# Performance work log

Hardware: AMD Instinct MI355X
Metric: run time of the kernel (lower is better)

The kernel has to match this reference:

```python
import jax, jax.numpy as jnp
import numpy as np

NUM_HEADS = 32
ROPE_BASE = 10000.0


def _rope_tables(seq_len, dim):
    inv_freq = 1.0 / (ROPE_BASE ** (jnp.arange(0, dim, 2, dtype=jnp.float32) / dim))
    t = jnp.arange(seq_len, dtype=jnp.float32)
    freqs = jnp.outer(t, inv_freq)                      # [S, dim/2]
    emb = jnp.concatenate([freqs, freqs], axis=-1)      # [S, dim]
    return jnp.cos(emb), jnp.sin(emb)


def _rotate_half(x):
    x1, x2 = jnp.split(x, 2, axis=-1)
    return jnp.concatenate([-x2, x1], axis=-1)


def setup_inputs() -> dict:
    key = jax.random.key(0)
    ks = jax.random.split(key, 5)
    B, T, C = 1, 4096, 4096
    hidden_states = jax.random.normal(ks[0], (B, T, C), dtype=jnp.float32)
    position_ids = jnp.arange(B * T, dtype=jnp.int64 if jax.config.jax_enable_x64 else jnp.int32).reshape(B, T)
    s = 0.02
    Wq = jax.random.normal(ks[1], (C, C), dtype=jnp.float32) * s
    Wk = jax.random.normal(ks[2], (C, C), dtype=jnp.float32) * s
    Wv = jax.random.normal(ks[3], (C, C), dtype=jnp.float32) * s
    Wo = jax.random.normal(ks[4], (C, C), dtype=jnp.float32) * s
    return {"hidden_states": hidden_states, "position_ids": position_ids,
            "Wq": Wq, "Wk": Wk, "Wv": Wv, "Wo": Wo}


def reference(hidden_states, position_ids, Wq, Wk, Wv, Wo):
    B, T, C = hidden_states.shape
    nh = NUM_HEADS
    hs = C // nh

    # Projections (torch Linear: x @ W.T), split heads -> [B, nh, T, hs]
    q = (hidden_states @ Wq.T).reshape(B, T, nh, hs).transpose(0, 2, 1, 3)
    k = (hidden_states @ Wk.T).reshape(B, T, nh, hs).transpose(0, 2, 1, 3)
    v = (hidden_states @ Wv.T).reshape(B, T, nh, hs).transpose(0, 2, 1, 3)

    # RoPE (prefill: kv_len == T)
    cos, sin = _rope_tables(T, hs)                      # [T, hs]
    cos_b = cos[position_ids][:, None]                  # [B, 1, T, hs]
    sin_b = sin[position_ids][:, None]
    q = q * cos_b + _rotate_half(q) * sin_b
    k = k * cos_b + _rotate_half(k) * sin_b

    # Eager attention with full [B, nh, T, T] scores (faithful to source)
    scale = hs ** -0.5
    attn = jnp.einsum("bhqd,bhkd->bhqk", q, k) * scale
    causal = jnp.tril(jnp.ones((T, T), dtype=bool))     # diagonal = kv_len - T = 0
    attn = jnp.where(causal[None, None], attn, -jnp.inf)
    attn = jax.nn.softmax(attn, axis=-1)
    out = jnp.einsum("bhqk,bhkd->bhqd", attn, v)
    out = out.transpose(0, 2, 1, 3).reshape(B, T, C)
    return out @ Wo.T
```

## Files before the change

### kernel.cpp

```cpp
#include <hip/hip_runtime.h>

typedef __attribute__((ext_vector_type(8))) short short8;
typedef __attribute__((ext_vector_type(4))) short short4v;
typedef __attribute__((ext_vector_type(4))) float f32x4;

#define NH 32
#define HS 128
#define CDIM 4096
#define QBLK 256
#define KVBLK 64
#define NQT 16

__device__ __forceinline__ ushort f2bf(float f) {
  union { float f; unsigned u; } a; a.f = f;
  unsigned u = a.u;
  return (ushort)((u + 0x7FFFu + ((u >> 16) & 1u)) >> 16);
}
__device__ __forceinline__ float bf2f(ushort h) {
  union { unsigned u; float f; } a; a.u = ((unsigned)h) << 16;
  return a.f;
}
__device__ __forceinline__ unsigned cvtpk_bf16(float lo, float hi) {
  unsigned r;
  asm("v_cvt_pk_bf16_f32 %0, %1, %2" : "=v"(r) : "v"(lo), "v"(hi));
  return r;
}

__device__ __forceinline__ void gld16(const void* g, void* l) {
  __builtin_amdgcn_global_load_lds((const __attribute__((address_space(1))) void*)g,
                                   (__attribute__((address_space(3))) void*)l, 16, 0, 0);
}

__device__ __forceinline__ unsigned lds_off(const void* p) {
  return (unsigned)(uintptr_t)(const __attribute__((address_space(3))) void*)p;
}

template<int OFF>
__device__ __forceinline__ short4v ds_tr16(unsigned addr) {
  short4v r;
  asm volatile("ds_read_b64_tr_b16 %0, %1 offset:%c2" : "=v"(r) : "v"(addr), "i"(OFF));
  return r;
}

__global__ __launch_bounds__(256) void cast_bf16_kernel(const float* __restrict__ in,
                                                        ushort* __restrict__ out, int n4) {
  int i = blockIdx.x * 256 + threadIdx.x;
  if (i >= n4) return;
  float4 v = ((const float4*)in)[i];
  ushort4 o;
  o.x = f2bf(v.x); o.y = f2bf(v.y); o.z = f2bf(v.z); o.w = f2bf(v.w);
  ((ushort4*)out)[i] = o;
}

#define A00 0
#define A01 16384
#define A10 32768
#define A11 49152
#define B00 65536
#define B01 81920
#define B10 98304
#define B11 114688

template<typename OutT>
__global__ __launch_bounds__(512, 2) void gemm256(const ushort* __restrict__ A,
                                                  const ushort* __restrict__ B,
                                                  OutT* __restrict__ C) {
  __shared__ char sm[131072];
  const int tid = threadIdx.x;
  const int w = tid >> 6, lane = tid & 63, lhi = lane >> 4, llo = lane & 15;

  const int bid = blockIdx.x;
  const int x = (bid & 7) * 32 + (bid >> 3);
  const int mt = x >> 4, nt = x & 15;
  const size_t m0 = (size_t)mt * 256, n0 = (size_t)nt * 256;

  const char* A0p = (const char*)(A + m0 * 4096);
  const char* A1p = A0p + 1048576;
  const char* B0p = (const char*)(B + n0 * 4096);
  const char* B1p = B0p + 1048576;

  const int i0 = tid, i1 = tid + 512;
  const int ri0 = i0 >> 3, ri1 = i1 >> 3;
  const int cg0 = (i0 & 7) ^ (((ri0 >> 2) & 1) << 1);
  const int cg1 = (i1 & 7) ^ (((ri1 >> 2) & 1) << 1);
  const int off0 = ri0 * 8192 + cg0 * 16;
  const int off1 = ri1 * 8192 + cg1 * 16;
  const unsigned sd0 = (unsigned)(w * 1024);
  const unsigned sd1 = (unsigned)(8192 + w * 1024);

  const int sw = ((llo >> 2) & 1) << 1;
  const unsigned rd0 = (unsigned)((llo * 8 + ((0 * 4 + lhi) ^ sw)) * 16);
  const unsigned rd1 = (unsigned)((llo * 8 + ((1 * 4 + lhi) ^ sw)) * 16);

  const int wmg = w >> 2, wng = w & 3;
  const unsigned aE = wmg ? A01 : A00;
  const unsigned aO = wmg ? A11 : A10;
  const unsigned bE = (wng >> 1) ? B01 : B00;
  const unsigned bO = (wng >> 1) ? B11 : B10;
  const unsigned bco = (unsigned)((wng & 1) * 8192);

  f32x4 acc[8][4] = {};
  short8 a0[4], a1[4], u0[2], u1[2], v0[2], v1[2];

#define STG(PAN, K0, LB) do { \
    gld16((PAN) + (size_t)(K0) * 2 + off0, sm + (LB) + sd0); \
    gld16((PAN) + (size_t)(K0) * 2 + off1, sm + (LB) + sd1); \
  } while (0)
#define LDA(BASE, MQ) do { _Pragma("unroll") for (int m_ = 0; m_ < 4; m_++) { \
    a0[m_] = *(const short8*)(sm + (BASE) + (MQ) * 8192 + m_ * 2048 + rd0); \
    a1[m_] = *(const short8*)(sm + (BASE) + (MQ) * 8192 + m_ * 2048 + rd1); } } while (0)
#define LDB(R0, R1, BASE, NQ) do { _Pragma("unroll") for (int n_ = 0; n_ < 2; n_++) { \
    R0[n_] = *(const short8*)(sm + (BASE) + bco + (NQ) * 4096 + n_ * 2048 + rd0); \
    R1[n_] = *(const short8*)(sm + (BASE) + bco + (NQ) * 4096 + n_ * 2048 + rd1); } } while (0)
#define MM(MQ, NQ, R0, R1) do { \
    _Pragma("unroll") for (int m_ = 0; m_ < 4; m_++) _Pragma("unroll") for (int n_ = 0; n_ < 2; n_++) \
      acc[(MQ) * 4 + m_][(NQ) * 2 + n_] = __builtin_amdgcn_mfma_f32_16x16x32_bf16(a0[m_], R0[n_], acc[(MQ) * 4 + m_][(NQ) * 2 + n_], 0, 0, 0); \
    _Pragma("unroll") for (int m_ = 0; m_ < 4; m_++) _Pragma("unroll") for (int n_ = 0; n_ < 2; n_++) \
      acc[(MQ) * 4 + m_][(NQ) * 2 + n_] = __builtin_amdgcn_mfma_f32_16x16x32_bf16(a1[m_], R1[n_], acc[(MQ) * 4 + m_][(NQ) * 2 + n_], 0, 0, 0); \
  } while (0)
#define BAR1 do { __builtin_amdgcn_s_barrier(); \
    asm volatile("s_waitcnt lgkmcnt(0)" ::: "memory"); \
    __builtin_amdgcn_sched_barrier(0); \
    __builtin_amdgcn_s_setprio(1); } while (0)
#define BAR2 do { __builtin_amdgcn_s_setprio(0); __builtin_amdgcn_s_barrier(); \
    __builtin_amdgcn_sched_barrier(0); } while (0)

  STG(B0p, 0, B00); STG(B1p, 0, B01); STG(A0p, 0, A00); STG(A1p, 0, A01);
  STG(B0p, 64, B10); STG(B1p, 64, B11); STG(A0p, 64, A10); STG(A1p, 64, A11);
  asm volatile("s_waitcnt vmcnt(8)" ::: "memory");
  __builtin_amdgcn_s_barrier();
  __builtin_amdgcn_sched_barrier(0);

  for (int it = 0; it < 32; ++it) {
    const int kc = it * 128;
    const bool st = (it < 31);
    LDA(aE, 0); LDB(u0, u1, bE, 0);
    BAR1; MM(0, 0, u0, u1); BAR2;
    LDB(v0, v1, bE, 1);
    BAR1; MM(0, 1, v0, v1); BAR2;
    LDA(aE, 1);
    if (st) STG(B0p, kc + 128, B00);
    BAR1; MM(1, 1, v0, v1); BAR2;
    if (st) { STG(B1p, kc + 128, B01); STG(A0p, kc + 128, A00); }
    BAR1; MM(1, 0, u0, u1);
    __builtin_amdgcn_s_setprio(0);
    if (st) asm volatile("s_waitcnt vmcnt(6)" ::: "memory");
    else    asm volatile("s_waitcnt vmcnt(0)" ::: "memory");
    __builtin_amdgcn_s_barrier();
    __builtin_amdgcn_sched_barrier(0);
    LDA(aO, 0); LDB(u0, u1, bO, 0);
    if (st) STG(A1p, kc + 128, A01);
    BAR1; MM(0, 0, u0, u1); BAR2;
    LDB(v0, v1, bO, 1);
    BAR1; MM(0, 1, v0, v1); BAR2;
    LDA(aO, 1);
    if (st) { STG(B0p, kc + 192, B10); STG(B1p, kc + 192, B11); }
    BAR1; MM(1, 1, v0, v1); BAR2;
    if (st) { STG(A0p, kc + 192, A10); STG(A1p, kc + 192, A11); }
    BAR1; MM(1, 0, u0, u1);
    __builtin_amdgcn_s_setprio(0);
    if (st) asm volatile("s_waitcnt vmcnt(8)" ::: "memory");
    __builtin_amdgcn_s_barrier();
    __builtin_amdgcn_sched_barrier(0);
  }

  const int wm = wmg * 128, wn = wng * 64;
#pragma unroll
  for (int m = 0; m < 8; m++) {
#pragma unroll
    for (int nf = 0; nf < 4; nf++) {
      const size_t col = n0 + wn + nf * 16 + llo;
#pragma unroll
      for (int j = 0; j < 4; j++) {
        const size_t row = m0 + wm + m * 16 + lhi * 4 + j;
        if constexpr (sizeof(OutT) == 4)
          C[row * 4096 + col] = acc[m][nf][j];
        else
          C[row * 4096 + col] = f2bf(acc[m][nf][j]);
      }
    }
  }
#undef STG
#undef LDA
#undef LDB
#undef MM
#undef BAR1
#undef BAR2
}

__global__ __launch_bounds__(256) void rope_kernel(ushort* __restrict__ Q,
                                                   ushort* __restrict__ Kb,
                                                   const int* __restrict__ pos_ids,
                                                   int nrows) {
  int gid = blockIdx.x * 256 + threadIdx.x;
  int d = gid & 63;
  int row = gid >> 6;
  if (row >= nrows) return;
  int t = row >> 5;
  int pos = pos_ids[t];
  float inv = expf((float)d * -0.14391156831212788f);
  float ang = (float)pos * inv;
  float s, c;
  sincosf(ang, &s, &c);
  size_t base = (size_t)row * HS;
  {
    float x1 = bf2f(Q[base + d]), x2 = bf2f(Q[base + d + 64]);
    Q[base + d]      = f2bf(x1 * c - x2 * s);
    Q[base + d + 64] = f2bf(x2 * c + x1 * s);
  }
  {
    float x1 = bf2f(Kb[base + d]), x2 = bf2f(Kb[base + d + 64]);
    Kb[base + d]      = f2bf(x1 * c - x2 * s);
    Kb[base + d + 64] = f2bf(x2 * c + x1 * s);
  }
}

__global__ __launch_bounds__(512) void flash_attn(const ushort* __restrict__ Q,
                                                  const ushort* __restrict__ K,
                                                  const ushort* __restrict__ V,
                                                  ushort* __restrict__ O) {
  __shared__ __align__(16) ushort Ks[KVBLK * HS];
  __shared__ __align__(16) ushort Vs[KVBLK * HS];
  __shared__ __align__(16) ushort Ps[8][32 * 72];
  const int tid = threadIdx.x;
  const int w = tid >> 6, l = tid & 63, lhi = l >> 4, llo = l & 15;
  const int qbp = blockIdx.x, h = blockIdx.y;

  const int g = llo >> 2, c = llo & 3;
  const int swz = g | ((lhi & 1) << 2);
  const int c1 = c >> 1;
  const int swL = swz & 1, swH = swz & 6;
  const unsigned trbase = lds_off(Vs) + (unsigned)((lhi * 8 + g) * 256 + ((c1 ^ swL) << 4) + (c & 1) * 8);

  const int srow = tid >> 4, sch = tid & 15;
  const int schK = sch ^ (srow & 7);
  const int schV = sch ^ ((srow & 3) | (((srow >> 3) & 1) << 2));

  char* pwB = (char*)Ps[w];
  const float scale = 0.08838834764831845f;

  short8 kreg[2], vreg[2];

  for (int ph = 0; ph < 2; ph++) {
    const int qt = ph ? (NQT - 1 - qbp) : qbp;
    const int qr0 = qt * QBLK + w * 32;
    const int ntile = 4 * qt + 4;

    short8 aq[2][4];
#pragma unroll
    for (int mf = 0; mf < 2; mf++) {
      const ushort* qp = Q + (size_t)(qr0 + mf * 16 + llo) * CDIM + h * HS + lhi * 8;
#pragma unroll
      for (int ki = 0; ki < 4; ki++) aq[mf][ki] = *(const short8*)(qp + ki * 32);
    }

    f32x4 acc[2][8] = {};
    float mrow[2] = {-1e30f, -1e30f};
    float lrow[2] = {0.f, 0.f};

#pragma unroll
    for (int r = 0; r < 2; r++) {
      const size_t rb = (size_t)(srow + r * 32) * CDIM + h * HS + sch * 8;
      kreg[r] = *(const short8*)(K + rb);
      vreg[r] = *(const short8*)(V + rb);
    }
#pragma unroll
    for (int r = 0; r < 2; r++) {
      const int row = srow + r * 32;
      *(short8*)((char*)Ks + ((row * 16 + schK) << 4)) = kreg[r];
      *(short8*)((char*)Vs + ((row * 16 + schV) << 4)) = vreg[r];
    }
    __syncthreads();

    for (int t = 0; t < ntile; t++) {
      const int kv0 = t * KVBLK;
      if (t + 1 < ntile) {
        const size_t rb = (size_t)(kv0 + KVBLK + srow) * CDIM + h * HS + sch * 8;
#pragma unroll
        for (int r = 0; r < 2; r++) {
          kreg[r] = *(const short8*)(K + rb + (size_t)r * 32 * CDIM);
          vreg[r] = *(const short8*)(V + rb + (size_t)r * 32 * CDIM);
        }
      }
      const bool active = (kv0 <= qr0 + 31);
      if (active) {
        f32x4 s[2][4];
        __builtin_amdgcn_s_setprio(1);
#pragma unroll
        for (int nt = 0; nt < 4; nt++) {
          const int krow = nt * 16 + llo;
          const char* kr = (const char*)Ks + krow * 256;
          short8 kf[4];
#pragma unroll
          for (int ki = 0; ki < 4; ki++)
            kf[ki] = *(const short8*)(kr + (((ki * 4 + lhi) ^ (krow & 7)) << 4));
          f32x4 s0 = {0.f, 0.f, 0.f, 0.f}, s1 = {0.f, 0.f, 0.f, 0.f};
#pragma unroll
          for (int ki = 0; ki < 4; ki++) {
            s0 = __builtin_amdgcn_mfma_f32_16x16x32_bf16(kf[ki], aq[0][ki], s0, 0, 0, 0);
            s1 = __builtin_amdgcn_mfma_f32_16x16x32_bf16(kf[ki], aq[1][ki], s1, 0, 0, 0);
          }
          s[0][nt] = s0; s[1][nt] = s1;
        }
        __builtin_amdgcn_s_setprio(0);

        short4v vl0[8], vh0[8];
#pragma unroll
        for (int on = 0; on < 8; on++) {
          unsigned a = trbase + (unsigned)(((on * 2) ^ swH) << 4);
          vl0[on] = ds_tr16<0>(a);
          vh0[on] = ds_tr16<1024>(a);
        }

        const bool needm = (kv0 + KVBLK - 1 > qr0);
#pragma unroll
        for (int mf = 0; mf < 2; mf++) {
          const int qi = qr0 + mf * 16 + llo;
#pragma unroll
          for (int nt = 0; nt < 4; nt++) {
            const int kvb = kv0 + nt * 16 + lhi * 4;
#pragma unroll
            for (int j = 0; j < 4; j++) {
              float sv = s[mf][nt][j] * scale;
              if (needm && kvb + j > qi) sv = -1e30f;
              s[mf][nt][j] = sv;
            }
          }
        }

#pragma unroll
        for (int mf = 0; mf < 2; mf++) {
          f32x4 mm;
#pragma unroll
          for (int j = 0; j < 4; j++)
            mm[j] = fmaxf(fmaxf(s[mf][0][j], s[mf][1][j]), fmaxf(s[mf][2][j], s[mf][3][j]));
          float pmax = fmaxf(fmaxf(mm[0], mm[1]), fmaxf(mm[2], mm[3]));
          pmax = fmaxf(pmax, __shfl_xor(pmax, 16));
          pmax = fmaxf(pmax, __shfl_xor(pmax, 32));
          if (__any(pmax > mrow[mf] + 8.f)) {
            float mn = fmaxf(mrow[mf], pmax);
            float sc = __expf(mrow[mf] - mn);
            mrow[mf] = mn;
            lrow[mf] *= sc;
#pragma unroll
            for (int on = 0; on < 8; on++)
#pragma unroll
              for (int j = 0; j < 4; j++) acc[mf][on][j] *= sc;
          }
          float rs = 0.f;
#pragma unroll
          for (int nt = 0; nt < 4; nt++) {
            float p0 = __expf(s[mf][nt][0] - mrow[mf]);
            float p1 = __expf(s[mf][nt][1] - mrow[mf]);
            float p2 = __expf(s[mf][nt][2] - mrow[mf]);
            float p3 = __expf(s[mf][nt][3] - mrow[mf]);
            rs += (p0 + p1) + (p2 + p3);
            uint2 pk;
            pk.x = cvtpk_bf16(p0, p1);
            pk.y = cvtpk_bf16(p2, p3);
            *(uint2*)(pwB + (mf * 16 + llo) * 144 + nt * 32 + lhi * 8) = pk;
          }
          rs += __shfl_xor(rs, 16);
          rs += __shfl_xor(rs, 32);
          lrow[mf] += rs;
        }

        {
          short8 pf0 = *(const short8*)(pwB + llo * 144 + lhi * 16);
          short8 pf1 = *(const short8*)(pwB + (16 + llo) * 144 + lhi * 16);
          asm volatile("s_waitcnt lgkmcnt(0)" ::: "memory");
          __builtin_amdgcn_sched_barrier(0);
          __builtin_amdgcn_s_setprio(1);
#pragma unroll
          for (int on = 0; on < 8; on++) {
            short8 vf = __builtin_shufflevector(vl0[on], vh0[on], 0, 1, 2, 3, 4, 5, 6, 7);
            acc[0][on] = __builtin_amdgcn_mfma_f32_16x16x32_bf16(vf, pf0, acc[0][on], 0, 0, 0);
            acc[1][on] = __builtin_amdgcn_mfma_f32_16x16x32_bf16(vf, pf1, acc[1][on], 0, 0, 0);
          }
          __builtin_amdgcn_s_setprio(0);
        }
        {
          short8 pf0 = *(const short8*)(pwB + llo * 144 + 64 + lhi * 16);
          short8 pf1 = *(const short8*)(pwB + (16 + llo) * 144 + 64 + lhi * 16);
          short4v vl[8], vh[8];
#pragma unroll
          for (int on = 0; on < 8; on++) {
            unsigned a = trbase + (unsigned)(((on * 2) ^ swH) << 4);
            vl[on] = ds_tr16<8192>(a);
            vh[on] = ds_tr16<9216>(a);
          }
          asm volatile("s_waitcnt lgkmcnt(0)" ::: "memory");
          __builtin_amdgcn_sched_barrier(0);
          __builtin_amdgcn_s_setprio(1);
#pragma unroll
          for (int on = 0; on < 8; on++) {
            short8 vf = __builtin_shufflevector(vl[on], vh[on], 0, 1, 2, 3, 4, 5, 6, 7);
            acc[0][on] = __builtin_amdgcn_mfma_f32_16x16x32_bf16(vf, pf0, acc[0][on], 0, 0, 0);
            acc[1][on] = __builtin_amdgcn_mfma_f32_16x16x32_bf16(vf, pf1, acc[1][on], 0, 0, 0);
          }
          __builtin_amdgcn_s_setprio(0);
        }
      }

      __syncthreads();
      if (t + 1 < ntile) {
#pragma unroll
        for (int r = 0; r < 2; r++) {
          const int row = srow + r * 32;
          *(short8*)((char*)Ks + ((row * 16 + schK) << 4)) = kreg[r];
          *(short8*)((char*)Vs + ((row * 16 + schV) << 4)) = vreg[r];
        }
      }
      __syncthreads();
    }

#pragma unroll
    for (int mf = 0; mf < 2; mf++) {
      const float ri = 1.0f / lrow[mf];
      ushort* orow = O + (size_t)(qr0 + mf * 16 + llo) * CDIM + h * HS + lhi * 4;
#pragma unroll
      for (int on = 0; on < 8; on++) {
        ushort4 o4;
        o4.x = f2bf(acc[mf][on][0] * ri);
        o4.y = f2bf(acc[mf][on][1] * ri);
        o4.z = f2bf(acc[mf][on][2] * ri);
        o4.w = f2bf(acc[mf][on][3] * ri);
        *(ushort4*)(orow + on * 16) = o4;
      }
    }
  }
}

extern "C" void kernel_launch(void* const* d_in, const int* in_sizes, int n_in,
                              void* d_out, int out_size, void* d_ws, size_t ws_size,
                              hipStream_t stream) {
  const float* hs = (const float*)d_in[0];
  const int* pos = (const int*)d_in[1];
  const float* Wq = (const float*)d_in[2];
  const float* Wk = (const float*)d_in[3];
  const float* Wv = (const float*)d_in[4];
  const float* Wo = (const float*)d_in[5];
  float* out = (float*)d_out;

  const int T = 4096;
  const size_t elems = (size_t)T * CDIM;

  ushort* hsb  = (ushort*)d_ws;
  ushort* wbuf = hsb + elems;
  ushort* qb   = wbuf + elems;
  ushort* kb   = qb + elems;
  ushort* vb   = kb + elems;
  ushort* attn = hsb;

  const int n4 = (int)(elems / 4);
  const int castBlocks = (n4 + 255) / 256;

  cast_bf16_kernel<<<castBlocks, 256, 0, stream>>>(hs, hsb, n4);

  cast_bf16_kernel<<<castBlocks, 256, 0, stream>>>(Wq, wbuf, n4);
  gemm256<ushort><<<256, 512, 0, stream>>>(hsb, wbuf, qb);

  cast_bf16_kernel<<<castBlocks, 256, 0, stream>>>(Wk, wbuf, n4);
  gemm256<ushort><<<256, 512, 0, stream>>>(hsb, wbuf, kb);

  cast_bf16_kernel<<<castBlocks, 256, 0, stream>>>(Wv, wbuf, n4);
  gemm256<ushort><<<256, 512, 0, stream>>>(hsb, wbuf, vb);

  rope_kernel<<<(T * NH * 64) / 256, 256, 0, stream>>>(qb, kb, pos, T * NH);

  flash_attn<<<dim3(NQT / 2, NH), 512, 0, stream>>>(qb, kb, vb, attn);

  cast_bf16_kernel<<<castBlocks, 256, 0, stream>>>(Wo, wbuf, n4);
  gemm256<float><<<256, 512, 0, stream>>>(attn, wbuf, out);
}
```

Measured before the change: 830.0 us.

## Split flash attention KV range across two blocks and merge with combine kernel

Flash attention now launches twice as many blocks along a new z dimension. Each block handles alternating KV tiles and writes its unnormalised partial output plus per-row max and sum statistics. A new combine kernel then merges the two partials with log-sum-exp weights, and the output buffer is reused as scratch space. This is meant to raise occupancy, since the grid of 256 blocks underfills the GPU, at the cost of extra global traffic, an extra launch, and bf16 rounding of the partial results. The GEMM also drops several sched_barrier calls, giving the compiler more scheduling freedom.

```diff
diff --git a/kernel.cpp b/kernel.cpp
--- a/kernel.cpp
+++ b/kernel.cpp
@@ -122,8 +122,7 @@
     asm volatile("s_waitcnt lgkmcnt(0)" ::: "memory"); \
     __builtin_amdgcn_sched_barrier(0); \
     __builtin_amdgcn_s_setprio(1); } while (0)
-#define BAR2 do { __builtin_amdgcn_s_setprio(0); __builtin_amdgcn_s_barrier(); \
-    __builtin_amdgcn_sched_barrier(0); } while (0)
+#define BAR2 do { __builtin_amdgcn_s_setprio(0); __builtin_amdgcn_s_barrier(); } while (0)
 
   STG(B0p, 0, B00); STG(B1p, 0, B01); STG(A0p, 0, A00); STG(A1p, 0, A01);
   STG(B0p, 64, B10); STG(B1p, 64, B11); STG(A0p, 64, A10); STG(A1p, 64, A11);
@@ -147,7 +146,6 @@
     if (st) asm volatile("s_waitcnt vmcnt(6)" ::: "memory");
     else    asm volatile("s_waitcnt vmcnt(0)" ::: "memory");
     __builtin_amdgcn_s_barrier();
-    __builtin_amdgcn_sched_barrier(0);
     LDA(aO, 0); LDB(u0, u1, bO, 0);
     if (st) STG(A1p, kc + 128, A01);
     BAR1; MM(0, 0, u0, u1); BAR2;
@@ -161,7 +159,6 @@
     __builtin_amdgcn_s_setprio(0);
     if (st) asm volatile("s_waitcnt vmcnt(8)" ::: "memory");
     __builtin_amdgcn_s_barrier();
-    __builtin_amdgcn_sched_barrier(0);
   }
 
   const int wm = wmg * 128, wn = wng * 64;
@@ -218,13 +215,18 @@
 __global__ __launch_bounds__(512) void flash_attn(const ushort* __restrict__ Q,
                                                   const ushort* __restrict__ K,
                                                   const ushort* __restrict__ V,
-                                                  ushort* __restrict__ O) {
+                                                  ushort* __restrict__ O0,
+                                                  ushort* __restrict__ O1,
+                                                  float2* __restrict__ ml0,
+                                                  float2* __restrict__ ml1) {
   __shared__ __align__(16) ushort Ks[KVBLK * HS];
   __shared__ __align__(16) ushort Vs[KVBLK * HS];
   __shared__ __align__(16) ushort Ps[8][32 * 72];
   const int tid = threadIdx.x;
   const int w = tid >> 6, l = tid & 63, lhi = l >> 4, llo = l & 15;
-  const int qbp = blockIdx.x, h = blockIdx.y;
+  const int qbp = blockIdx.x, h = blockIdx.y, z = blockIdx.z;
+  ushort* __restrict__ Op = z ? O1 : O0;
+  float2* __restrict__ mlp = z ? ml1 : ml0;
 
   const int g = llo >> 2, c = llo & 3;
   const int swz = g | ((lhi & 1) << 2);
@@ -260,7 +262,7 @@
 
 #pragma unroll
     for (int r = 0; r < 2; r++) {
-      const size_t rb = (size_t)(srow + r * 32) * CDIM + h * HS + sch * 8;
+      const size_t rb = (size_t)(z * KVBLK + srow + r * 32) * CDIM + h * HS + sch * 8;
       kreg[r] = *(const short8*)(K + rb);
       vreg[r] = *(const short8*)(V + rb);
     }
@@ -272,10 +274,10 @@
     }
     __syncthreads();
 
-    for (int t = 0; t < ntile; t++) {
+    for (int t = z; t < ntile; t += 2) {
       const int kv0 = t * KVBLK;
-      if (t + 1 < ntile) {
-        const size_t rb = (size_t)(kv0 + KVBLK + srow) * CDIM + h * HS + sch * 8;
+      if (t + 2 < ntile) {
+        const size_t rb = (size_t)(kv0 + 2 * KVBLK + srow) * CDIM + h * HS + sch * 8;
 #pragma unroll
         for (int r = 0; r < 2; r++) {
           kreg[r] = *(const short8*)(K + rb + (size_t)r * 32 * CDIM);
@@ -403,7 +405,7 @@
       }
 
       __syncthreads();
-      if (t + 1 < ntile) {
+      if (t + 2 < ntile) {
 #pragma unroll
         for (int r = 0; r < 2; r++) {
           const int row = srow + r * 32;
@@ -416,19 +418,47 @@
 
 #pragma unroll
     for (int mf = 0; mf < 2; mf++) {
-      const float ri = 1.0f / lrow[mf];
-      ushort* orow = O + (size_t)(qr0 + mf * 16 + llo) * CDIM + h * HS + lhi * 4;
+      const int q = qr0 + mf * 16 + llo;
+      if (lhi == 0) {
+        float2 v2; v2.x = mrow[mf]; v2.y = lrow[mf];
+        mlp[(size_t)h * 4096 + q] = v2;
+      }
+      ushort* orow = Op + (size_t)q * CDIM + h * HS + lhi * 4;
 #pragma unroll
       for (int on = 0; on < 8; on++) {
         ushort4 o4;
-        o4.x = f2bf(acc[mf][on][0] * ri);
-        o4.y = f2bf(acc[mf][on][1] * ri);
-        o4.z = f2bf(acc[mf][on][2] * ri);
-        o4.w = f2bf(acc[mf][on][3] * ri);
+        o4.x = f2bf(acc[mf][on][0]);
+        o4.y = f2bf(acc[mf][on][1]);
+        o4.z = f2bf(acc[mf][on][2]);
+        o4.w = f2bf(acc[mf][on][3]);
         *(ushort4*)(orow + on * 16) = o4;
       }
     }
   }
+}
+
+__global__ __launch_bounds__(256) void combine_kernel(ushort* __restrict__ O0,
+                                                      const ushort* __restrict__ O1,
+                                                      const float2* __restrict__ ml0,
+                                                      const float2* __restrict__ ml1) {
+  int cch = blockIdx.x * 256 + threadIdx.x;
+  int q = cch >> 9;
+  int h = (cch >> 4) & 31;
+  int x = cch & 15;
+  size_t off = (size_t)q * CDIM + h * HS + x * 8;
+  float2 a = ml0[h * 4096 + q];
+  float2 b = ml1[h * 4096 + q];
+  float m = fmaxf(a.x, b.x);
+  float w0 = __expf(a.x - m), w1 = __expf(b.x - m);
+  float inv = 1.0f / (w0 * a.y + w1 * b.y);
+  w0 *= inv; w1 *= inv;
+  short8 u = *(const short8*)(O0 + off);
+  short8 v = *(const short8*)(O1 + off);
+  short8 r;
+#pragma unroll
+  for (int j = 0; j < 8; j++)
+    r[j] = (short)f2bf(bf2f((ushort)u[j]) * w0 + bf2f((ushort)v[j]) * w1);
+  *(short8*)(O0 + off) = r;
 }
 
 extern "C" void kernel_launch(void* const* d_in, const int* in_sizes, int n_in,
@@ -450,7 +480,10 @@
   ushort* qb   = wbuf + elems;
   ushort* kb   = qb + elems;
   ushort* vb   = kb + elems;
-  ushort* attn = hsb;
+
+  ushort* O1  = (ushort*)d_out;
+  float2* ml0 = (float2*)((char*)d_out + 33554432);
+  float2* ml1 = ml0 + (size_t)NH * T;
 
   const int n4 = (int)(elems / 4);
   const int castBlocks = (n4 + 255) / 256;
@@ -468,8 +501,9 @@
 
   rope_kernel<<<(T * NH * 64) / 256, 256, 0, stream>>>(qb, kb, pos, T * NH);
 
-  flash_attn<<<dim3(NQT / 2, NH), 512, 0, stream>>>(qb, kb, vb, attn);
+  flash_attn<<<dim3(NQT / 2, NH, 2), 512, 0, stream>>>(qb, kb, vb, hsb, O1, ml0, ml1);
+  combine_kernel<<<(T * NH * 16) / 256, 256, 0, stream>>>(hsb, O1, ml0, ml1);
 
   cast_bf16_kernel<<<castBlocks, 256, 0, stream>>>(Wo, wbuf, n4);
-  gemm256<float><<<256, 512, 0, stream>>>(attn, wbuf, out);
-}
+  gemm256<float><<<256, 512, 0, stream>>>(hsb, wbuf, out);
+}
```

Result: slower. 859.6 us (+3.6%).

## Use 16 waves of 16 query rows in flash attention, relax GEMM sched barriers

Applied to the files above, without the earlier changes.

The flash attention kernel moves from 8 waves each handling 32 query rows to 16 waves (1024 threads) each handling 16 rows. Each thread now loads a single K/V row chunk into LDS per tile. This raises the wave count per block and lowers register pressure per wave, at the cost of reusing each loaded K/V fragment over fewer query rows. Separately, several sched_barrier fences in the GEMM main loop are removed so the compiler can reorder instructions around the barriers.

```diff
diff --git a/kernel.cpp b/kernel.cpp
--- a/kernel.cpp
+++ b/kernel.cpp
@@ -122,8 +122,7 @@
     asm volatile("s_waitcnt lgkmcnt(0)" ::: "memory"); \
     __builtin_amdgcn_sched_barrier(0); \
     __builtin_amdgcn_s_setprio(1); } while (0)
-#define BAR2 do { __builtin_amdgcn_s_setprio(0); __builtin_amdgcn_s_barrier(); \
-    __builtin_amdgcn_sched_barrier(0); } while (0)
+#define BAR2 do { __builtin_amdgcn_s_setprio(0); __builtin_amdgcn_s_barrier(); } while (0)
 
   STG(B0p, 0, B00); STG(B1p, 0, B01); STG(A0p, 0, A00); STG(A1p, 0, A01);
   STG(B0p, 64, B10); STG(B1p, 64, B11); STG(A0p, 64, A10); STG(A1p, 64, A11);
@@ -147,7 +146,6 @@
     if (st) asm volatile("s_waitcnt vmcnt(6)" ::: "memory");
     else    asm volatile("s_waitcnt vmcnt(0)" ::: "memory");
     __builtin_amdgcn_s_barrier();
-    __builtin_amdgcn_sched_barrier(0);
     LDA(aO, 0); LDB(u0, u1, bO, 0);
     if (st) STG(A1p, kc + 128, A01);
     BAR1; MM(0, 0, u0, u1); BAR2;
@@ -161,7 +159,6 @@
     __builtin_amdgcn_s_setprio(0);
     if (st) asm volatile("s_waitcnt vmcnt(8)" ::: "memory");
     __builtin_amdgcn_s_barrier();
-    __builtin_amdgcn_sched_barrier(0);
   }
 
   const int wm = wmg * 128, wn = wng * 64;
@@ -215,13 +212,13 @@
   }
 }
 
-__global__ __launch_bounds__(512) void flash_attn(const ushort* __restrict__ Q,
-                                                  const ushort* __restrict__ K,
-                                                  const ushort* __restrict__ V,
-                                                  ushort* __restrict__ O) {
+__global__ __launch_bounds__(1024) void flash_attn(const ushort* __restrict__ Q,
+                                                   const ushort* __restrict__ K,
+                                                   const ushort* __restrict__ V,
+                                                   ushort* __restrict__ O) {
   __shared__ __align__(16) ushort Ks[KVBLK * HS];
   __shared__ __align__(16) ushort Vs[KVBLK * HS];
-  __shared__ __align__(16) ushort Ps[8][32 * 72];
+  __shared__ __align__(16) ushort Ps[16][16 * 72];
   const int tid = threadIdx.x;
   const int w = tid >> 6, l = tid & 63, lhi = l >> 4, llo = l & 15;
   const int qbp = blockIdx.x, h = blockIdx.y;
@@ -239,36 +236,30 @@
   char* pwB = (char*)Ps[w];
   const float scale = 0.08838834764831845f;
 
-  short8 kreg[2], vreg[2];
+  short8 kreg, vreg;
 
   for (int ph = 0; ph < 2; ph++) {
     const int qt = ph ? (NQT - 1 - qbp) : qbp;
-    const int qr0 = qt * QBLK + w * 32;
+    const int qr0 = qt * QBLK + w * 16;
     const int ntile = 4 * qt + 4;
 
-    short8 aq[2][4];
-#pragma unroll
-    for (int mf = 0; mf < 2; mf++) {
-      const ushort* qp = Q + (size_t)(qr0 + mf * 16 + llo) * CDIM + h * HS + lhi * 8;
-#pragma unroll
-      for (int ki = 0; ki < 4; ki++) aq[mf][ki] = *(const short8*)(qp + ki * 32);
+    short8 aq[4];
+    {
+      const ushort* qp = Q + (size_t)(qr0 + llo) * CDIM + h * HS + lhi * 8;
+#pragma unroll
+      for (int ki = 0; ki < 4; ki++) aq[ki] = *(const short8*)(qp + ki * 32);
     }
 
-    f32x4 acc[2][8] = {};
-    float mrow[2] = {-1e30f, -1e30f};
-    float lrow[2] = {0.f, 0.f};
-
-#pragma unroll
-    for (int r = 0; r < 2; r++) {
-      const size_t rb = (size_t)(srow + r * 32) * CDIM + h * HS + sch * 8;
-      kreg[r] = *(const short8*)(K + rb);
-      vreg[r] = *(const short8*)(V + rb);
-    }
-#pragma unroll
-    for (int r = 0; r < 2; r++) {
-      const int row = srow + r * 32;
-      *(short8*)((char*)Ks + ((row * 16 + schK) << 4)) = kreg[r];
-      *(short8*)((char*)Vs + ((row * 16 + schV) << 4)) = vreg[r];
+    f32x4 acc[8] = {};
+    float mrow = -1e30f;
+    float lrow = 0.f;
+
+    {
+      const size_t rb = (size_t)srow * CDIM + h * HS + sch * 8;
+      kreg = *(const short8*)(K + rb);
+      vreg = *(const short8*)(V + rb);
+      *(short8*)((char*)Ks + ((srow * 16 + schK) << 4)) = kreg;
+      *(short8*)((char*)Vs + ((srow * 16 + schV) << 4)) = vreg;
     }
     __syncthreads();
 
@@ -276,15 +267,12 @@
       const int kv0 = t * KVBLK;
       if (t + 1 < ntile) {
         const size_t rb = (size_t)(kv0 + KVBLK + srow) * CDIM + h * HS + sch * 8;
-#pragma unroll
-        for (int r = 0; r < 2; r++) {
-          kreg[r] = *(const short8*)(K + rb + (size_t)r * 32 * CDIM);
-          vreg[r] = *(const short8*)(V + rb + (size_t)r * 32 * CDIM);
-        }
+        kreg = *(const short8*)(K + rb);
+        vreg = *(const short8*)(V + rb);
       }
-      const bool active = (kv0 <= qr0 + 31);
+      const bool active = (kv0 <= qr0 + 15);
       if (active) {
-        f32x4 s[2][4];
+        f32x4 s[4];
         __builtin_amdgcn_s_setprio(1);
 #pragma unroll
         for (int nt = 0; nt < 4; nt++) {
@@ -294,94 +282,84 @@
 #pragma unroll
           for (int ki = 0; ki < 4; ki++)
             kf[ki] = *(const short8*)(kr + (((ki * 4 + lhi) ^ (krow & 7)) << 4));
-          f32x4 s0 = {0.f, 0.f, 0.f, 0.f}, s1 = {0.f, 0.f, 0.f, 0.f};
-#pragma unroll
-          for (int ki = 0; ki < 4; ki++) {
-            s0 = __builtin_amdgcn_mfma_f32_16x16x32_bf16(kf[ki], aq[0][ki], s0, 0, 0, 0);
-            s1 = __builtin_amdgcn_mfma_f32_16x16x32_bf16(kf[ki], aq[1][ki], s1, 0, 0, 0);
-          }
-          s[0][nt] = s0; s[1][nt] = s1;
+          f32x4 s0 = {0.f, 0.f, 0.f, 0.f};
+#pragma unroll
+          for (int ki = 0; ki < 4; ki++)
+            s0 = __builtin_amdgcn_mfma_f32_16x16x32_bf16(kf[ki], aq[ki], s0, 0, 0, 0);
+          s[nt] = s0;
         }
         __builtin_amdgcn_s_setprio(0);
 
-        short4v vl0[8], vh0[8];
-#pragma unroll
-        for (int on = 0; on < 8; on++) {
-          unsigned a = trbase + (unsigned)(((on * 2) ^ swH) << 4);
-          vl0[on] = ds_tr16<0>(a);
-          vh0[on] = ds_tr16<1024>(a);
+        const bool needm = (kv0 + KVBLK - 1 > qr0);
+        const int qi = qr0 + llo;
+#pragma unroll
+        for (int nt = 0; nt < 4; nt++) {
+          const int kvb = kv0 + nt * 16 + lhi * 4;
+#pragma unroll
+          for (int j = 0; j < 4; j++) {
+            float sv = s[nt][j] * scale;
+            if (needm && kvb + j > qi) sv = -1e30f;
+            s[nt][j] = sv;
+          }
         }
 
-        const bool needm = (kv0 + KVBLK - 1 > qr0);
-#pragma unroll
-        for (int mf = 0; mf < 2; mf++) {
-          const int qi = qr0 + mf * 16 + llo;
-#pragma unroll
-          for (int nt = 0; nt < 4; nt++) {
-            const int kvb = kv0 + nt * 16 + lhi * 4;
-#pragma unroll
-            for (int j = 0; j < 4; j++) {
-              float sv = s[mf][nt][j] * scale;
-              if (needm && kvb + j > qi) sv = -1e30f;
-              s[mf][nt][j] = sv;
-            }
-          }
-        }
-
-#pragma unroll
-        for (int mf = 0; mf < 2; mf++) {
+        {
           f32x4 mm;
 #pragma unroll
           for (int j = 0; j < 4; j++)
-            mm[j] = fmaxf(fmaxf(s[mf][0][j], s[mf][1][j]), fmaxf(s[mf][2][j], s[mf][3][j]));
+            mm[j] = fmaxf(fmaxf(s[0][j], s[1][j]), fmaxf(s[2][j], s[3][j]));
           float pmax = fmaxf(fmaxf(mm[0], mm[1]), fmaxf(mm[2], mm[3]));
           pmax = fmaxf(pmax, __shfl_xor(pmax, 16));
           pmax = fmaxf(pmax, __shfl_xor(pmax, 32));
-          if (__any(pmax > mrow[mf] + 8.f)) {
-            float mn = fmaxf(mrow[mf], pmax);
-            float sc = __expf(mrow[mf] - mn);
-            mrow[mf] = mn;
-            lrow[mf] *= sc;
+          if (__any(pmax > mrow + 8.f)) {
+            float mn = fmaxf(mrow, pmax);
+            float sc = __expf(mrow - mn);
+            mrow = mn;
+            lrow *= sc;
 #pragma unroll
             for (int on = 0; on < 8; on++)
 #pragma unroll
-              for (int j = 0; j < 4; j++) acc[mf][on][j] *= sc;
+              for (int j = 0; j < 4; j++) acc[on][j] *= sc;
           }
           float rs = 0.f;
 #pragma unroll
           for (int nt = 0; nt < 4; nt++) {
-            float p0 = __expf(s[mf][nt][0] - mrow[mf]);
-            float p1 = __expf(s[mf][nt][1] - mrow[mf]);
-            float p2 = __expf(s[mf][nt][2] - mrow[mf]);
-            float p3 = __expf(s[mf][nt][3] - mrow[mf]);
+            float p0 = __expf(s[nt][0] - mrow);
+            float p1 = __expf(s[nt][1] - mrow);
+            float p2 = __expf(s[nt][2] - mrow);
+            float p3 = __expf(s[nt][3] - mrow);
             rs += (p0 + p1) + (p2 + p3);
             uint2 pk;
             pk.x = cvtpk_bf16(p0, p1);
             pk.y = cvtpk_bf16(p2, p3);
-            *(uint2*)(pwB + (mf * 16 + llo) * 144 + nt * 32 + lhi * 8) = pk;
+            *(uint2*)(pwB + llo * 144 + nt * 32 + lhi * 8) = pk;
           }
           rs += __shfl_xor(rs, 16);
           rs += __shfl_xor(rs, 32);
-          lrow[mf] += rs;
+          lrow += rs;
         }
 
         {
-          short8 pf0 = *(const short8*)(pwB + llo * 144 + lhi * 16);
-          short8 pf1 = *(const short8*)(pwB + (16 + llo) * 144 + lhi * 16);
+          short8 pf = *(const short8*)(pwB + llo * 144 + lhi * 16);
+          short4v vl[8], vh[8];
+#pragma unroll
+          for (int on = 0; on < 8; on++) {
+            unsigned a = trbase + (unsigned)(((on * 2) ^ swH) << 4);
+            vl[on] = ds_tr16<0>(a);
+            vh[on] = ds_tr16<1024>(a);
+          }
           asm volatile("s_waitcnt lgkmcnt(0)" ::: "memory");
           __builtin_amdgcn_sched_barrier(0);
           __builtin_amdgcn_s_setprio(1);
 #pragma unroll
           for (int on = 0; on < 8; on++) {
-            short8 vf = __builtin_shufflevector(vl0[on], vh0[on], 0, 1, 2, 3, 4, 5, 6, 7);
-            acc[0][on] = __builtin_amdgcn_mfma_f32_16x16x32_bf16(vf, pf0, acc[0][on], 0, 0, 0);
-            acc[1][on] = __builtin_amdgcn_mfma_f32_16x16x32_bf16(vf, pf1, acc[1][on], 0, 0, 0);
+            short8 vf = __builtin_shufflevector(vl[on], vh[on], 0, 1, 2, 3, 4, 5, 6, 7);
+            acc[on] = __builtin_amdgcn_mfma_f32_16x16x32_bf16(vf, pf, acc[on], 0, 0, 0);
           }
           __builtin_amdgcn_s_setprio(0);
         }
         {
-          short8 pf0 = *(const short8*)(pwB + llo * 144 + 64 + lhi * 16);
-          short8 pf1 = *(const short8*)(pwB + (16 + llo) * 144 + 64 + lhi * 16);
+          short8 pf = *(const short8*)(pwB + llo * 144 + 64 + lhi * 16);
           short4v vl[8], vh[8];
 #pragma unroll
           for (int on = 0; on < 8; on++) {
@@ -395,8 +373,7 @@
 #pragma unroll
           for (int on = 0; on < 8; on++) {
             short8 vf = __builtin_shufflevector(vl[on], vh[on], 0, 1, 2, 3, 4, 5, 6, 7);
-            acc[0][on] = __builtin_amdgcn_mfma_f32_16x16x32_bf16(vf, pf0, acc[0][on], 0, 0, 0);
-            acc[1][on] = __builtin_amdgcn_mfma_f32_16x16x32_bf16(vf, pf1, acc[1][on], 0, 0, 0);
+            acc[on] = __builtin_amdgcn_mfma_f32_16x16x32_bf16(vf, pf, acc[on], 0, 0, 0);
           }
           __builtin_amdgcn_s_setprio(0);
         }
@@ -404,27 +381,22 @@
 
       __syncthreads();
       if (t + 1 < ntile) {
-#pragma unroll
-        for (int r = 0; r < 2; r++) {
-          const int row = srow + r * 32;
-          *(short8*)((char*)Ks + ((row * 16 + schK) << 4)) = kreg[r];
-          *(short8*)((char*)Vs + ((row * 16 + schV) << 4)) = vreg[r];
-        }
+        *(short8*)((char*)Ks + ((srow * 16 + schK) << 4)) = kreg;
+        *(short8*)((char*)Vs + ((srow * 16 + schV) << 4)) = vreg;
       }
       __syncthreads();
     }
 
-#pragma unroll
-    for (int mf = 0; mf < 2; mf++) {
-      const float ri = 1.0f / lrow[mf];
-      ushort* orow = O + (size_t)(qr0 + mf * 16 + llo) * CDIM + h * HS + lhi * 4;
+    {
+      const float ri = 1.0f / lrow;
+      ushort* orow = O + (size_t)(qr0 + llo) * CDIM + h * HS + lhi * 4;
 #pragma unroll
       for (int on = 0; on < 8; on++) {
         ushort4 o4;
-        o4.x = f2bf(acc[mf][on][0] * ri);
-        o4.y = f2bf(acc[mf][on][1] * ri);
-        o4.z = f2bf(acc[mf][on][2] * ri);
-        o4.w = f2bf(acc[mf][on][3] * ri);
+        o4.x = f2bf(acc[on][0] * ri);
+        o4.y = f2bf(acc[on][1] * ri);
+        o4.z = f2bf(acc[on][2] * ri);
+        o4.w = f2bf(acc[on][3] * ri);
         *(ushort4*)(orow + on * 16) = o4;
       }
     }
@@ -450,7 +422,6 @@
   ushort* qb   = wbuf + elems;
   ushort* kb   = qb + elems;
   ushort* vb   = kb + elems;
-  ushort* attn = hsb;
 
   const int n4 = (int)(elems / 4);
   const int castBlocks = (n4 + 255) / 256;
@@ -468,8 +439,8 @@
 
   rope_kernel<<<(T * NH * 64) / 256, 256, 0, stream>>>(qb, kb, pos, T * NH);
 
-  flash_attn<<<dim3(NQT / 2, NH), 512, 0, stream>>>(qb, kb, vb, attn);
+  flash_attn<<<dim3(NQT / 2, NH), 1024, 0, stream>>>(qb, kb, vb, hsb);
 
   cast_bf16_kernel<<<castBlocks, 256, 0, stream>>>(Wo, wbuf, n4);
-  gemm256<float><<<256, 512, 0, stream>>>(attn, wbuf, out);
-}
+  gemm256<float><<<256, 512, 0, stream>>>(hsb, wbuf, out);
+}
```

New measurement: 829.9 us. Within noise of the previous version (-0.0%).

## Split KV tile across wave pairs in flash attention and merge partial softmax

Applied to the files above, without the earlier changes.

The flash attention block goes from 8 to 16 waves, each pair splitting every 64-row KV tile into two 32-row halves. Each wave keeps its own running max, sum and partial output, and the halves are combined at the end through LDS exchange buffers. The combine stores the second half's partial output as bf16, which adds some rounding error, and extra barriers and LDS use may limit occupancy. The GEMM also drops several sched_barrier fences so the compiler can move instructions across the pipeline barriers.

```diff
diff --git a/kernel.cpp b/kernel.cpp
--- a/kernel.cpp
+++ b/kernel.cpp
@@ -122,8 +122,7 @@
     asm volatile("s_waitcnt lgkmcnt(0)" ::: "memory"); \
     __builtin_amdgcn_sched_barrier(0); \
     __builtin_amdgcn_s_setprio(1); } while (0)
-#define BAR2 do { __builtin_amdgcn_s_setprio(0); __builtin_amdgcn_s_barrier(); \
-    __builtin_amdgcn_sched_barrier(0); } while (0)
+#define BAR2 do { __builtin_amdgcn_s_setprio(0); __builtin_amdgcn_s_barrier(); } while (0)
 
   STG(B0p, 0, B00); STG(B1p, 0, B01); STG(A0p, 0, A00); STG(A1p, 0, A01);
   STG(B0p, 64, B10); STG(B1p, 64, B11); STG(A0p, 64, A10); STG(A1p, 64, A11);
@@ -147,7 +146,6 @@
     if (st) asm volatile("s_waitcnt vmcnt(6)" ::: "memory");
     else    asm volatile("s_waitcnt vmcnt(0)" ::: "memory");
     __builtin_amdgcn_s_barrier();
-    __builtin_amdgcn_sched_barrier(0);
     LDA(aO, 0); LDB(u0, u1, bO, 0);
     if (st) STG(A1p, kc + 128, A01);
     BAR1; MM(0, 0, u0, u1); BAR2;
@@ -161,7 +159,6 @@
     __builtin_amdgcn_s_setprio(0);
     if (st) asm volatile("s_waitcnt vmcnt(8)" ::: "memory");
     __builtin_amdgcn_s_barrier();
-    __builtin_amdgcn_sched_barrier(0);
   }
 
   const int wm = wmg * 128, wn = wng * 64;
@@ -215,35 +212,39 @@
   }
 }
 
-__global__ __launch_bounds__(512) void flash_attn(const ushort* __restrict__ Q,
-                                                  const ushort* __restrict__ K,
-                                                  const ushort* __restrict__ V,
-                                                  ushort* __restrict__ O) {
+__global__ __launch_bounds__(1024) void flash_attn(const ushort* __restrict__ Q,
+                                                   const ushort* __restrict__ K,
+                                                   const ushort* __restrict__ V,
+                                                   ushort* __restrict__ O) {
   __shared__ __align__(16) ushort Ks[KVBLK * HS];
   __shared__ __align__(16) ushort Vs[KVBLK * HS];
-  __shared__ __align__(16) ushort Ps[8][32 * 72];
+  __shared__ __align__(16) char PsB[16 * 2304];
+  __shared__ __align__(16) char Xch[8 * 8448];
+  __shared__ float2 mlX[8][32];
   const int tid = threadIdx.x;
   const int w = tid >> 6, l = tid & 63, lhi = l >> 4, llo = l & 15;
+  const int qg = w >> 1, kg = w & 1;
   const int qbp = blockIdx.x, h = blockIdx.y;
 
   const int g = llo >> 2, c = llo & 3;
   const int swz = g | ((lhi & 1) << 2);
   const int c1 = c >> 1;
   const int swL = swz & 1, swH = swz & 6;
-  const unsigned trbase = lds_off(Vs) + (unsigned)((lhi * 8 + g) * 256 + ((c1 ^ swL) << 4) + (c & 1) * 8);
+  const unsigned trbase = lds_off(Vs) + (unsigned)((lhi * 8 + g) * 256 + ((c1 ^ swL) << 4) + (c & 1) * 8 + kg * 8192);
 
   const int srow = tid >> 4, sch = tid & 15;
   const int schK = sch ^ (srow & 7);
   const int schV = sch ^ ((srow & 3) | (((srow >> 3) & 1) << 2));
 
-  char* pwB = (char*)Ps[w];
+  char* pwB = PsB + w * 2304;
+  char* xg = Xch + qg * 8448;
   const float scale = 0.08838834764831845f;
 
-  short8 kreg[2], vreg[2];
+  short8 kreg, vreg;
 
   for (int ph = 0; ph < 2; ph++) {
     const int qt = ph ? (NQT - 1 - qbp) : qbp;
-    const int qr0 = qt * QBLK + w * 32;
+    const int qr0 = qt * QBLK + qg * 32;
     const int ntile = 4 * qt + 4;
 
     short8 aq[2][4];
@@ -258,17 +259,12 @@
     float mrow[2] = {-1e30f, -1e30f};
     float lrow[2] = {0.f, 0.f};
 
-#pragma unroll
-    for (int r = 0; r < 2; r++) {
-      const size_t rb = (size_t)(srow + r * 32) * CDIM + h * HS + sch * 8;
-      kreg[r] = *(const short8*)(K + rb);
-      vreg[r] = *(const short8*)(V + rb);
-    }
-#pragma unroll
-    for (int r = 0; r < 2; r++) {
-      const int row = srow + r * 32;
-      *(short8*)((char*)Ks + ((row * 16 + schK) << 4)) = kreg[r];
-      *(short8*)((char*)Vs + ((row * 16 + schV) << 4)) = vreg[r];
+    {
+      const size_t rb = (size_t)srow * CDIM + h * HS + sch * 8;
+      kreg = *(const short8*)(K + rb);
+      vreg = *(const short8*)(V + rb);
+      *(short8*)((char*)Ks + ((srow * 16 + schK) << 4)) = kreg;
+      *(short8*)((char*)Vs + ((srow * 16 + schV) << 4)) = vreg;
     }
     __syncthreads();
 
@@ -276,19 +272,17 @@
       const int kv0 = t * KVBLK;
       if (t + 1 < ntile) {
         const size_t rb = (size_t)(kv0 + KVBLK + srow) * CDIM + h * HS + sch * 8;
-#pragma unroll
-        for (int r = 0; r < 2; r++) {
-          kreg[r] = *(const short8*)(K + rb + (size_t)r * 32 * CDIM);
-          vreg[r] = *(const short8*)(V + rb + (size_t)r * 32 * CDIM);
-        }
-      }
-      const bool active = (kv0 <= qr0 + 31);
+        kreg = *(const short8*)(K + rb);
+        vreg = *(const short8*)(V + rb);
+      }
+      const int kvh = kv0 + kg * 32;
+      const bool active = (kvh <= qr0 + 31);
       if (active) {
-        f32x4 s[2][4];
+        f32x4 s[2][2];
         __builtin_amdgcn_s_setprio(1);
 #pragma unroll
-        for (int nt = 0; nt < 4; nt++) {
-          const int krow = nt * 16 + llo;
+        for (int nt = 0; nt < 2; nt++) {
+          const int krow = kg * 32 + nt * 16 + llo;
           const char* kr = (const char*)Ks + krow * 256;
           short8 kf[4];
 #pragma unroll
@@ -304,21 +298,13 @@
         }
         __builtin_amdgcn_s_setprio(0);
 
-        short4v vl0[8], vh0[8];
-#pragma unroll
-        for (int on = 0; on < 8; on++) {
-          unsigned a = trbase + (unsigned)(((on * 2) ^ swH) << 4);
-          vl0[on] = ds_tr16<0>(a);
-          vh0[on] = ds_tr16<1024>(a);
-        }
-
-        const bool needm = (kv0 + KVBLK - 1 > qr0);
+        const bool needm = (kvh + 31 > qr0);
 #pragma unroll
         for (int mf = 0; mf < 2; mf++) {
           const int qi = qr0 + mf * 16 + llo;
 #pragma unroll
-          for (int nt = 0; nt < 4; nt++) {
-            const int kvb = kv0 + nt * 16 + lhi * 4;
+          for (int nt = 0; nt < 2; nt++) {
+            const int kvb = kvh + nt * 16 + lhi * 4;
 #pragma unroll
             for (int j = 0; j < 4; j++) {
               float sv = s[mf][nt][j] * scale;
@@ -332,8 +318,7 @@
         for (int mf = 0; mf < 2; mf++) {
           f32x4 mm;
 #pragma unroll
-          for (int j = 0; j < 4; j++)
-            mm[j] = fmaxf(fmaxf(s[mf][0][j], s[mf][1][j]), fmaxf(s[mf][2][j], s[mf][3][j]));
+          for (int j = 0; j < 4; j++) mm[j] = fmaxf(s[mf][0][j], s[mf][1][j]);
           float pmax = fmaxf(fmaxf(mm[0], mm[1]), fmaxf(mm[2], mm[3]));
           pmax = fmaxf(pmax, __shfl_xor(pmax, 16));
           pmax = fmaxf(pmax, __shfl_xor(pmax, 32));
@@ -349,7 +334,7 @@
           }
           float rs = 0.f;
 #pragma unroll
-          for (int nt = 0; nt < 4; nt++) {
+          for (int nt = 0; nt < 2; nt++) {
             float p0 = __expf(s[mf][nt][0] - mrow[mf]);
             float p1 = __expf(s[mf][nt][1] - mrow[mf]);
             float p2 = __expf(s[mf][nt][2] - mrow[mf]);
@@ -358,7 +343,7 @@
             uint2 pk;
             pk.x = cvtpk_bf16(p0, p1);
             pk.y = cvtpk_bf16(p2, p3);
-            *(uint2*)(pwB + (mf * 16 + llo) * 144 + nt * 32 + lhi * 8) = pk;
+            *(uint2*)(pwB + (mf * 16 + llo) * 72 + nt * 32 + lhi * 8) = pk;
           }
           rs += __shfl_xor(rs, 16);
           rs += __shfl_xor(rs, 32);
@@ -366,28 +351,14 @@
         }
 
         {
-          short8 pf0 = *(const short8*)(pwB + llo * 144 + lhi * 16);
-          short8 pf1 = *(const short8*)(pwB + (16 + llo) * 144 + lhi * 16);
-          asm volatile("s_waitcnt lgkmcnt(0)" ::: "memory");
-          __builtin_amdgcn_sched_barrier(0);
-          __builtin_amdgcn_s_setprio(1);
-#pragma unroll
-          for (int on = 0; on < 8; on++) {
-            short8 vf = __builtin_shufflevector(vl0[on], vh0[on], 0, 1, 2, 3, 4, 5, 6, 7);
-            acc[0][on] = __builtin_amdgcn_mfma_f32_16x16x32_bf16(vf, pf0, acc[0][on], 0, 0, 0);
-            acc[1][on] = __builtin_amdgcn_mfma_f32_16x16x32_bf16(vf, pf1, acc[1][on], 0, 0, 0);
-          }
-          __builtin_amdgcn_s_setprio(0);
-        }
-        {
-          short8 pf0 = *(const short8*)(pwB + llo * 144 + 64 + lhi * 16);
-          short8 pf1 = *(const short8*)(pwB + (16 + llo) * 144 + 64 + lhi * 16);
+          short8 pf0 = *(const short8*)(pwB + llo * 72 + lhi * 16);
+          short8 pf1 = *(const short8*)(pwB + (16 + llo) * 72 + lhi * 16);
           short4v vl[8], vh[8];
 #pragma unroll
           for (int on = 0; on < 8; on++) {
             unsigned a = trbase + (unsigned)(((on * 2) ^ swH) << 4);
-            vl[on] = ds_tr16<8192>(a);
-            vh[on] = ds_tr16<9216>(a);
+            vl[on] = ds_tr16<0>(a);
+            vh[on] = ds_tr16<1024>(a);
           }
           asm volatile("s_waitcnt lgkmcnt(0)" ::: "memory");
           __builtin_amdgcn_sched_barrier(0);
@@ -404,30 +375,55 @@
 
       __syncthreads();
       if (t + 1 < ntile) {
-#pragma unroll
-        for (int r = 0; r < 2; r++) {
-          const int row = srow + r * 32;
-          *(short8*)((char*)Ks + ((row * 16 + schK) << 4)) = kreg[r];
-          *(short8*)((char*)Vs + ((row * 16 + schV) << 4)) = vreg[r];
-        }
+        *(short8*)((char*)Ks + ((srow * 16 + schK) << 4)) = kreg;
+        *(short8*)((char*)Vs + ((srow * 16 + schV) << 4)) = vreg;
       }
       __syncthreads();
     }
 
-#pragma unroll
-    for (int mf = 0; mf < 2; mf++) {
-      const float ri = 1.0f / lrow[mf];
-      ushort* orow = O + (size_t)(qr0 + mf * 16 + llo) * CDIM + h * HS + lhi * 4;
-#pragma unroll
-      for (int on = 0; on < 8; on++) {
-        ushort4 o4;
-        o4.x = f2bf(acc[mf][on][0] * ri);
-        o4.y = f2bf(acc[mf][on][1] * ri);
-        o4.z = f2bf(acc[mf][on][2] * ri);
-        o4.w = f2bf(acc[mf][on][3] * ri);
-        *(ushort4*)(orow + on * 16) = o4;
-      }
-    }
+    if (kg == 1) {
+#pragma unroll
+      for (int mf = 0; mf < 2; mf++) {
+        if (lhi == 0) {
+          float2 v2; v2.x = mrow[mf]; v2.y = lrow[mf];
+          mlX[qg][mf * 16 + llo] = v2;
+        }
+        char* xr = xg + (mf * 16 + llo) * 264 + lhi * 8;
+#pragma unroll
+        for (int on = 0; on < 8; on++) {
+          ushort4 o4;
+          o4.x = f2bf(acc[mf][on][0]);
+          o4.y = f2bf(acc[mf][on][1]);
+          o4.z = f2bf(acc[mf][on][2]);
+          o4.w = f2bf(acc[mf][on][3]);
+          *(ushort4*)(xr + on * 32) = o4;
+        }
+      }
+    }
+    __syncthreads();
+    if (kg == 0) {
+#pragma unroll
+      for (int mf = 0; mf < 2; mf++) {
+        float2 o = mlX[qg][mf * 16 + llo];
+        float m = fmaxf(mrow[mf], o.x);
+        float w0 = __expf(mrow[mf] - m), w1 = __expf(o.x - m);
+        float ri = 1.0f / (w0 * lrow[mf] + w1 * o.y);
+        w0 *= ri; w1 *= ri;
+        const char* xr = xg + (mf * 16 + llo) * 264 + lhi * 8;
+        ushort* orow = O + (size_t)(qr0 + mf * 16 + llo) * CDIM + h * HS + lhi * 4;
+#pragma unroll
+        for (int on = 0; on < 8; on++) {
+          ushort4 px = *(const ushort4*)(xr + on * 32);
+          ushort4 o4;
+          o4.x = f2bf(acc[mf][on][0] * w0 + bf2f(px.x) * w1);
+          o4.y = f2bf(acc[mf][on][1] * w0 + bf2f(px.y) * w1);
+          o4.z = f2bf(acc[mf][on][2] * w0 + bf2f(px.z) * w1);
+          o4.w = f2bf(acc[mf][on][3] * w0 + bf2f(px.w) * w1);
+          *(ushort4*)(orow + on * 16) = o4;
+        }
+      }
+    }
+    __syncthreads();
   }
 }
 
@@ -450,7 +446,6 @@
   ushort* qb   = wbuf + elems;
   ushort* kb   = qb + elems;
   ushort* vb   = kb + elems;
-  ushort* attn = hsb;
 
   const int n4 = (int)(elems / 4);
   const int castBlocks = (n4 + 255) / 256;
@@ -468,8 +463,8 @@
 
   rope_kernel<<<(T * NH * 64) / 256, 256, 0, stream>>>(qb, kb, pos, T * NH);
 
-  flash_attn<<<dim3(NQT / 2, NH), 512, 0, stream>>>(qb, kb, vb, attn);
+  flash_attn<<<dim3(NQT / 2, NH), 1024, 0, stream>>>(qb, kb, vb, hsb);
 
   cast_bf16_kernel<<<castBlocks, 256, 0, stream>>>(Wo, wbuf, n4);
-  gemm256<float><<<256, 512, 0, stream>>>(attn, wbuf, out);
-}
+  gemm256<float><<<256, 512, 0, stream>>>(hsb, wbuf, out);
+}
```

After: 1.520 ms. +83.1%, slower.
